# Performance work log

Measured on AMD Instinct MI355X. Metric: run time of the kernel, lower is better.

## Reference

```python
import jax, jax.numpy as jnp
import numpy as np

SEQ = 2048
D_MODEL = 2048
N_HEADS = 16
D_HEAD = D_MODEL // N_HEADS
GN_EPS = 1e-5


def apply_xpos(x, inv=False, base=10000.0, scale_base=512.0):
    # x: (sqlen, d_head). Standard xPos: rotary embedding with exponential length scale.
    s, d = x.shape
    half = d // 2
    freqs = 1.0 / (base ** (jnp.arange(half, dtype=jnp.float32) / half))
    pos = jnp.arange(s, dtype=jnp.float32)
    ang = pos[:, None] * freqs[None, :]                       # (s, half)
    sin, cos = jnp.sin(ang), jnp.cos(ang)
    scale = ((jnp.arange(half, dtype=jnp.float32) + 0.4 * d) / (1.4 * d)) ** (pos[:, None] / scale_base)
    if inv:
        scale = 1.0 / scale
    x1, x2 = x[:, :half], x[:, half:]
    y1 = (x1 * cos - x2 * sin) * scale
    y2 = (x1 * sin + x2 * cos) * scale
    return jnp.concatenate([y1, y2], axis=-1)


def setup_inputs() -> dict:
    key = jax.random.key(0)
    ks = jax.random.split(key, 8)
    s = D_MODEL ** -0.5
    return {
        "x": jax.random.normal(ks[0], (SEQ, D_MODEL), jnp.float32),
        "state": jax.random.normal(ks[1], (N_HEADS, D_HEAD, D_HEAD), jnp.float32) * 0.1,
        "Wqkv": jax.random.normal(ks[2], (3 * D_MODEL, D_MODEL), jnp.float32) * s,
        "Walpha": jax.random.normal(ks[3], (1, D_MODEL), jnp.float32) * s,
        "gn_w": jnp.ones((D_MODEL,), jnp.float32),
        "gn_b": jnp.zeros((D_MODEL,), jnp.float32),
        "Wgate": jax.random.normal(ks[4], (D_MODEL, D_MODEL), jnp.float32) * s,
        "Wout": jax.random.normal(ks[5], (D_MODEL, D_MODEL), jnp.float32) * s,
    }


def reference(x, state, Wqkv, Walpha, gn_w, gn_b, Wgate, Wout):
    sqlen = x.shape[0]
    # qkv projection -> (3, H, s, Dh)
    qkv = (x @ Wqkv.T).reshape(sqlen, 3, N_HEADS, D_HEAD).transpose(1, 2, 0, 3)
    q, k, v = qkv[0], qkv[1], qkv[2]
    q = jax.vmap(apply_xpos)(q)
    k = jax.vmap(lambda t: apply_xpos(t, inv=True))(k)

    alphas = -jnp.log1p(jnp.exp(-(x @ Walpha.T)))             # log-sigmoid, (s, 1)
    k = (1.0 - jnp.exp(alphas)) * k                            # broadcast (s,1) over (H,s,Dh)
    a = jnp.cumsum(alphas, axis=0)                             # (s, 1)

    # Decay matrix; mask BEFORE exp (equivalent to tril-after since upper is zeroed,
    # but avoids overflow in exp for the upper triangle).
    tril = jnp.tril(jnp.ones((sqlen, sqlen), bool))
    Delta = jnp.exp(jnp.where(tril, a - a.T, -jnp.inf))        # (s, s)

    attn = jnp.tril(jnp.einsum('hid,hjd,ij->hij', q, k, Delta))  # (H, s, s)
    ret = jnp.einsum('hij,hjd->ihd', attn, v)                    # (s, H, Dh)

    new_state = jnp.exp(a[-1]) * state                           # (H, Dh, Dh)
    ret = ret + jnp.einsum('hid,hde->ihe', q, new_state)
    new_state = new_state + jnp.einsum('hid,hie,i->hde', k, v, jnp.exp(a[::-1, 0]))

    # GroupNorm(n_heads groups) over d_model, per token
    r = ret.reshape(sqlen, N_HEADS, D_HEAD)
    mu = r.mean(-1, keepdims=True)
    var = r.var(-1, keepdims=True)
    r = (r - mu) * jax.lax.rsqrt(var + GN_EPS)
    ret = r.reshape(sqlen, D_MODEL) * gn_w + gn_b

    gate = jax.nn.swish(ret @ Wgate.T)
    out = (gate * ret) @ Wout.T
    return out, new_state
```

## Files before the change

kernel.cpp:

```cpp
#include <hip/hip_runtime.h>

#define SEQ 2048
#define DM 2048
#define NH 16
#define DH 128

typedef float f32x4 __attribute__((ext_vector_type(4)));
typedef short s16x8 __attribute__((ext_vector_type(8)));

__device__ __forceinline__ ushort f2bf(float f) {
    unsigned u = __builtin_bit_cast(unsigned, f);
    return (ushort)((u + 0x7FFFu + ((u >> 16) & 1u)) >> 16);
}
__device__ __forceinline__ float bf2f(ushort u) {
    return __builtin_bit_cast(float, (unsigned)u << 16);
}
__device__ __forceinline__ void gload_lds16(const void* g, void* l) {
    __builtin_amdgcn_global_load_lds((const __attribute__((address_space(1))) void*)g,
                                     (__attribute__((address_space(3))) void*)l, 16, 0, 0);
}

__global__ __launch_bounds__(256) void k_prep1(const float* __restrict__ x,
                                               const float* __restrict__ wal,
                                               ushort* __restrict__ x_bf,
                                               float* __restrict__ z,
                                               const float* __restrict__ Wqkv,
                                               ushort* __restrict__ Wqkv_bf,
                                               float* __restrict__ tsin,
                                               float* __restrict__ tcos,
                                               float* __restrict__ tsc) {
    int b = blockIdx.x, t = threadIdx.x;
    if (b < SEQ) {
        const float4* xr = (const float4*)(x + (size_t)b * DM);
        const float4* wa = (const float4*)wal;
        float4 v0 = xr[t], v1 = xr[t + 256];
        float4 w0 = wa[t], w1 = wa[t + 256];
        float s = v0.x * w0.x + v0.y * w0.y + v0.z * w0.z + v0.w * w0.w
                + v1.x * w1.x + v1.y * w1.y + v1.z * w1.z + v1.w * w1.w;
        ushort4 o0, o1;
        o0.x = f2bf(v0.x); o0.y = f2bf(v0.y); o0.z = f2bf(v0.z); o0.w = f2bf(v0.w);
        o1.x = f2bf(v1.x); o1.y = f2bf(v1.y); o1.z = f2bf(v1.z); o1.w = f2bf(v1.w);
        ushort4* xb = (ushort4*)(x_bf + (size_t)b * DM);
        xb[t] = o0; xb[t + 256] = o1;
        __shared__ float red[4];
        int lane = t & 63, wv = t >> 6;
        #pragma unroll
        for (int off = 32; off; off >>= 1) s += __shfl_down(s, off);
        if (lane == 0) red[wv] = s;
        __syncthreads();
        if (t == 0) z[b] = red[0] + red[1] + red[2] + red[3];
    } else if (b < SEQ + 3 * DM * DM / 4 / 256) {
        int i = (b - SEQ) * 256 + t;
        float4 v = ((const float4*)Wqkv)[i];
        ushort4 o;
        o.x = f2bf(v.x); o.y = f2bf(v.y); o.z = f2bf(v.z); o.w = f2bf(v.w);
        ((ushort4*)Wqkv_bf)[i] = o;
    } else {
        int idx = (b - SEQ - 3 * DM * DM / 4 / 256) * 256 + t;
        int i = idx >> 6, j = idx & 63;
        float freq = powf(10000.f, -(float)j / 64.f);
        float ang = (float)i * freq;
        tsin[idx] = sinf(ang);
        tcos[idx] = cosf(ang);
        tsc[idx]  = powf(((float)j + 51.2f) / 179.2f, (float)i / 512.f);
    }
}

__global__ __launch_bounds__(256) void k_scan(const float* __restrict__ z,
                                              float* __restrict__ a,
                                              float* __restrict__ wrev,
                                              float* __restrict__ kscale,
                                              float* __restrict__ exp_alast) {
    __shared__ float sh[SEQ];
    __shared__ float csum[256];
    int t = threadIdx.x;
    for (int i = t; i < SEQ; i += 256) {
        float al = -log1pf(expf(-z[i]));
        sh[i] = al;
        kscale[i] = 1.f - expf(al);
    }
    __syncthreads();
    int base = t * 8;
    float run = 0.f, loc[8];
    #pragma unroll
    for (int j = 0; j < 8; j++) { run += sh[base + j]; loc[j] = run; }
    csum[t] = run;
    __syncthreads();
    if (t == 0) {
        float r = 0.f;
        for (int i = 0; i < 256; i++) { float v = csum[i]; csum[i] = r; r += v; }
    }
    __syncthreads();
    float off = csum[t];
    #pragma unroll
    for (int j = 0; j < 8; j++) { float av = loc[j] + off; sh[base + j] = av; a[base + j] = av; }
    __syncthreads();
    for (int i = t; i < SEQ; i += 256) wrev[i] = expf(sh[SEQ - 1 - i]);
    if (t == 0) *exp_alast = expf(sh[SEQ - 1]);
}

template <int EPI, int STORE_BF16>
__global__ __launch_bounds__(256) void k_gemm_mfma(
    const ushort* __restrict__ A,
    const ushort* __restrict__ B,
    void* __restrict__ Cv, int ldc,
    const ushort* __restrict__ aux,
    int K)
{
    __shared__ __align__(16) ushort As[128 * 32];
    __shared__ __align__(16) ushort Bs[128 * 32];
    int bx = blockIdx.x, by = blockIdx.y;
    int nwg = gridDim.x * gridDim.y;
    if ((nwg & 7) == 0) {
        int id = by * gridDim.x + bx;
        int cpx = nwg >> 3;
        int swz = (id & 7) * cpx + (id >> 3);
        bx = swz % gridDim.x; by = swz / gridDim.x;
    }
    int bm = by * 128, bn = bx * 128;
    int tid = threadIdx.x;
    int w = tid >> 6, l = tid & 63;
    int wr = w >> 1, wc = w & 1;
    int lr = l & 15, kg = l >> 4;

    int srow = w * 16 + (l >> 2);
    int scol = (l & 3) * 8;
    const ushort* ga0 = A + (size_t)(bm + srow) * K + scol;
    const ushort* ga1 = A + (size_t)(bm + 64 + srow) * K + scol;
    const ushort* gb0 = B + (size_t)(bn + srow) * K + scol;
    const ushort* gb1 = B + (size_t)(bn + 64 + srow) * K + scol;
    ushort* la0 = As + w * 512;
    ushort* la1 = As + 2048 + w * 512;
    ushort* lb0 = Bs + w * 512;
    ushort* lb1 = Bs + 2048 + w * 512;

    f32x4 acc[4][4] = {};

    for (int k0 = 0; k0 < K; k0 += 32) {
        __syncthreads();
        gload_lds16(ga0 + k0, la0);
        gload_lds16(ga1 + k0, la1);
        gload_lds16(gb0 + k0, lb0);
        gload_lds16(gb1 + k0, lb1);
        __syncthreads();

        s16x8 af[4], bfr[4];
        #pragma unroll
        for (int m = 0; m < 4; m++)
            af[m] = *(const s16x8*)(As + (wr * 64 + m * 16 + lr) * 32 + kg * 8);
        #pragma unroll
        for (int n = 0; n < 4; n++)
            bfr[n] = *(const s16x8*)(Bs + (wc * 64 + n * 16 + lr) * 32 + kg * 8);
        #pragma unroll
        for (int m = 0; m < 4; m++)
            #pragma unroll
            for (int n = 0; n < 4; n++)
                asm volatile("v_mfma_f32_16x16x32_bf16 %0, %1, %2, %0"
                             : "+v"(acc[m][n]) : "v"(af[m]), "v"(bfr[n]));
    }
    asm volatile("s_nop 7\n\ts_nop 7\n\ts_nop 7" ::: );

    #pragma unroll
    for (int m = 0; m < 4; m++) {
        int grow = bm + wr * 64 + m * 16 + kg * 4;
        #pragma unroll
        for (int n = 0; n < 4; n++) {
            int gcol = bn + wc * 64 + n * 16 + lr;
            #pragma unroll
            for (int j = 0; j < 4; j++) {
                float c = acc[m][n][j];
                size_t off = (size_t)(grow + j) * ldc + gcol;
                if (EPI == 1) {
                    float sig = 1.f / (1.f + __expf(-c));
                    c = c * sig * bf2f(aux[off]);
                }
                if (STORE_BF16) ((ushort*)Cv)[off] = f2bf(c);
                else            ((float*)Cv)[off] = c;
            }
        }
    }
}

__global__ __launch_bounds__(256) void k_gemm_qkv(
    const ushort* __restrict__ A,
    const ushort* __restrict__ B,
    const float* __restrict__ tsin,
    const float* __restrict__ tcos,
    const float* __restrict__ tsc,
    const float* __restrict__ kscale,
    const float* __restrict__ wrev,
    ushort* __restrict__ qh,
    ushort* __restrict__ kh,
    ushort* __restrict__ vth,
    ushort* __restrict__ kwtr)
{
    __shared__ __align__(16) char smem[34816];
    ushort* As = (ushort*)smem;
    ushort* Bs = (ushort*)(smem + 8192);
    const int K = DM;
    int bx = blockIdx.x, by = blockIdx.y;
    {
        int id = by * gridDim.x + bx;
        int cpx = (gridDim.x * gridDim.y) >> 3;
        int swz = (id & 7) * cpx + (id >> 3);
        bx = swz % gridDim.x; by = swz / gridDim.x;
    }
    int bm = by * 128, bn = bx * 128;
    int tid = threadIdx.x;
    int w = tid >> 6, l = tid & 63;
    int wr = w >> 1, wc = w & 1;
    int lr = l & 15, kg = l >> 4;

    int srow = w * 16 + (l >> 2);
    int scol = (l & 3) * 8;
    const ushort* ga0 = A + (size_t)(bm + srow) * K + scol;
    const ushort* ga1 = A + (size_t)(bm + 64 + srow) * K + scol;
    const ushort* gb0 = B + (size_t)(bn + srow) * K + scol;
    const ushort* gb1 = B + (size_t)(bn + 64 + srow) * K + scol;
    ushort* la0 = As + w * 512;
    ushort* la1 = As + 2048 + w * 512;
    ushort* lb0 = Bs + w * 512;
    ushort* lb1 = Bs + 2048 + w * 512;

    f32x4 acc[4][4] = {};

    for (int k0 = 0; k0 < K; k0 += 32) {
        __syncthreads();
        gload_lds16(ga0 + k0, la0);
        gload_lds16(ga1 + k0, la1);
        gload_lds16(gb0 + k0, lb0);
        gload_lds16(gb1 + k0, lb1);
        __syncthreads();

        s16x8 af[4], bfr[4];
        #pragma unroll
        for (int m = 0; m < 4; m++)
            af[m] = *(const s16x8*)(As + (wr * 64 + m * 16 + lr) * 32 + kg * 8);
        #pragma unroll
        for (int n = 0; n < 4; n++)
            bfr[n] = *(const s16x8*)(Bs + (wc * 64 + n * 16 + lr) * 32 + kg * 8);
        #pragma unroll
        for (int m = 0; m < 4; m++)
            #pragma unroll
            for (int n = 0; n < 4; n++)
                asm volatile("v_mfma_f32_16x16x32_bf16 %0, %1, %2, %0"
                             : "+v"(acc[m][n]) : "v"(af[m]), "v"(bfr[n]));
    }
    asm volatile("s_nop 7\n\ts_nop 7\n\ts_nop 7" ::: );

    __syncthreads();
    ushort* S = (ushort*)smem;
    #pragma unroll
    for (int m = 0; m < 4; m++) {
        int row = wr * 64 + m * 16 + kg * 4;
        #pragma unroll
        for (int n = 0; n < 4; n++) {
            int col = wc * 64 + n * 16 + lr;
            #pragma unroll
            for (int j = 0; j < 4; j++)
                S[(row + j) * 129 + col] = f2bf(acc[m][n][j]);
        }
    }
    __syncthreads();

    int type = bn >> 11;
    int h = (bn & 2047) >> 7;

    if (type < 2) {
        #pragma unroll 4
        for (int rr = 0; rr < 32; rr++) {
            int r = w * 32 + rr;
            int i = bm + r;
            float sn = tsin[i * 64 + l], cs = tcos[i * 64 + l], sc = tsc[i * 64 + l];
            float v1 = bf2f(S[r * 129 + l]), v2 = bf2f(S[r * 129 + l + 64]);
            float r1 = v1 * cs - v2 * sn, r2 = v1 * sn + v2 * cs;
            size_t ob = ((size_t)h * SEQ + i) * DH;
            if (type == 0) {
                qh[ob + l]      = f2bf(r1 * sc);
                qh[ob + l + 64] = f2bf(r2 * sc);
            } else {
                float ks = kscale[i], wv = wrev[i];
                float isc = 1.f / sc;
                float k1 = r1 * isc * ks, k2 = r2 * isc * ks;
                kh[ob + l]      = f2bf(k1);
                kh[ob + l + 64] = f2bf(k2);
                S[r * 129 + l]      = f2bf(k1 * wv);
                S[r * 129 + l + 64] = f2bf(k2 * wv);
            }
        }
    }
    if (type >= 1) {
        __syncthreads();
        ushort* dstT = (type == 1) ? kwtr : vth;
        #pragma unroll 4
        for (int dd = 0; dd < 32; dd++) {
            int d = w * 32 + dd;
            ushort2 o;
            o.x = S[(2 * l) * 129 + d];
            o.y = S[(2 * l + 1) * 129 + d];
            *(ushort2*)(dstT + ((size_t)h * DH + d) * SEQ + bm + 2 * l) = o;
        }
    }
}

#define NUNITS 48
__constant__ unsigned char U_QT[NUNITS] = {
    31,31,30,15, 30,29,29,28,14, 28,27,27,26,13, 26,25,25,24,12,
    24,23,23,22,11, 22,21,21,20,10, 20,19,19,18,9, 18,17,17,16,8,
    16,7,6,5,4,3,2,1,0};
__constant__ unsigned char U_T0[NUNITS] = {
    0,16,0,0, 16,0,15,0,0, 15,0,14,0,0, 14,0,13,0,0,
    13,0,12,0,0, 12,0,11,0,0, 11,0,10,0,0, 10,0,9,0,0,
    9,0,0,0,0,0,0,0,0};
__constant__ unsigned char U_T1[NUNITS] = {
    16,32,16,16, 31,15,30,15,15, 29,14,28,14,14, 27,13,26,13,13,
    25,12,24,12,12, 23,11,22,11,11, 21,10,20,10,10, 19,9,18,9,9,
    17,8,7,6,5,4,3,2,1};

__global__ __launch_bounds__(256) void k_attn_mega(
    const ushort* __restrict__ qh,
    const ushort* __restrict__ kh,
    const ushort* __restrict__ vth,
    const ushort* __restrict__ kwtr,
    const float* __restrict__ a,
    float* __restrict__ ret,
    float* __restrict__ ret2,
    float* __restrict__ part,
    const float* __restrict__ Wgate,
    ushort* __restrict__ Wgate_bf,
    const float* __restrict__ Wout,
    ushort* __restrict__ Wout_bf)
{
    __shared__ __align__(16) char smem[81920];
    int h = blockIdx.x, u = blockIdx.y;
    int tid = threadIdx.x;
    int w = tid >> 6, l = tid & 63;
    int lr = l & 15, kg = l >> 4;

    if (u >= 56) {
        int id = (u - 56) * NH + h;
        const float4* g0 = (const float4*)Wgate;
        const float4* g1 = (const float4*)Wout;
        #pragma unroll 4
        for (int it = 0; it < 32; it++) {
            int idx = id * 8192 + it * 256 + tid;
            float4 v = g0[idx];
            ushort4 o;
            o.x = f2bf(v.x); o.y = f2bf(v.y); o.z = f2bf(v.z); o.w = f2bf(v.w);
            ((ushort4*)Wgate_bf)[idx] = o;
            v = g1[idx];
            o.x = f2bf(v.x); o.y = f2bf(v.y); o.z = f2bf(v.z); o.w = f2bf(v.w);
            ((ushort4*)Wout_bf)[idx] = o;
        }
        return;
    }
    if (u >= 48) {
        int ch = u - 48;
        const ushort* A = kwtr + (size_t)h * DH * SEQ + ch * (SEQ / 8);
        const ushort* B = vth  + (size_t)h * DH * SEQ + ch * (SEQ / 8);
        ushort* As = (ushort*)smem;
        ushort* Bs = (ushort*)(smem + 8192);
        int wr = w >> 1, wc = w & 1;
        int srow = w * 16 + (l >> 2);
        int scol = (l & 3) * 8;
        const ushort* ga0 = A + (size_t)srow * SEQ + scol;
        const ushort* ga1 = A + (size_t)(64 + srow) * SEQ + scol;
        const ushort* gb0 = B + (size_t)srow * SEQ + scol;
        const ushort* gb1 = B + (size_t)(64 + srow) * SEQ + scol;
        ushort* la0 = As + w * 512;
        ushort* la1 = As + 2048 + w * 512;
        ushort* lb0 = Bs + w * 512;
        ushort* lb1 = Bs + 2048 + w * 512;
        f32x4 acc[4][4] = {};
        for (int k0 = 0; k0 < SEQ / 8; k0 += 32) {
            __syncthreads();
            gload_lds16(ga0 + k0, la0);
            gload_lds16(ga1 + k0, la1);
            gload_lds16(gb0 + k0, lb0);
            gload_lds16(gb1 + k0, lb1);
            __syncthreads();
            s16x8 af[4], bfr[4];
            #pragma unroll
            for (int m = 0; m < 4; m++)
                af[m] = *(const s16x8*)(As + (wr * 64 + m * 16 + lr) * 32 + kg * 8);
            #pragma unroll
            for (int n = 0; n < 4; n++)
                bfr[n] = *(const s16x8*)(Bs + (wc * 64 + n * 16 + lr) * 32 + kg * 8);
            #pragma unroll
            for (int m = 0; m < 4; m++)
                #pragma unroll
                for (int n = 0; n < 4; n++)
                    asm volatile("v_mfma_f32_16x16x32_bf16 %0, %1, %2, %0"
                                 : "+v"(acc[m][n]) : "v"(af[m]), "v"(bfr[n]));
        }
        asm volatile("s_nop 7\n\ts_nop 7\n\ts_nop 7" ::: );
        float* p = part + ((size_t)ch * NH + h) * DH * DH;
        #pragma unroll
        for (int m = 0; m < 4; m++) {
            int grow = wr * 64 + m * 16 + kg * 4;
            #pragma unroll
            for (int n = 0; n < 4; n++) {
                int gcol = wc * 64 + n * 16 + lr;
                #pragma unroll
                for (int j = 0; j < 4; j++)
                    p[(size_t)(grow + j) * DH + gcol] = acc[m][n][j];
            }
        }
        return;
    }

    int qt = U_QT[u], t0 = U_T0[u], t1 = U_T1[u];
    int i0 = qt * 64;
    const ushort* Q  = qh  + (size_t)h * SEQ * DH;
    const ushort* K  = kh  + (size_t)h * SEQ * DH;
    const ushort* Vt = vth + (size_t)h * DH * SEQ;
#define KS(B) ((ushort*)(smem + (B) * 16384))
#define VS(B) ((ushort*)(smem + 32768 + (B) * 16384))
    char* Ps = smem + 65536;
    float* a_lds = (float*)(smem + 73728);

    int span = t1 * 64;
    for (int i = tid; i < span; i += 256) a_lds[i] = a[i];

    s16x8 qf[4];
    #pragma unroll
    for (int c = 0; c < 4; c++)
        qf[c] = *(const s16x8*)(Q + (size_t)(i0 + w * 16 + lr) * DH + c * 32 + kg * 8);
    float aq[4];
    #pragma unroll
    for (int r = 0; r < 4; r++) aq[r] = a[i0 + w * 16 + kg * 4 + r];

    f32x4 oacc[8] = {};

#define STAGE(T, B) do { int j0_ = (T) * 64;                                      \
    _Pragma("unroll") for (int g = 0; g < 4; g++) {                               \
        int row = w * 16 + g * 4 + (l >> 4);                                      \
        int cb = ((l & 15) * 16) ^ ((row & 7) << 4);                              \
        gload_lds16(K + (size_t)(j0_ + row) * DH + cb / 2,                        \
                    (char*)KS(B) + (w * 16 + g * 4) * 256); }                     \
    _Pragma("unroll") for (int g = 0; g < 4; g++) {                               \
        int e = w * 32 + g * 8 + (l >> 3);                                        \
        int cb = ((l & 7) * 16) ^ ((e & 7) << 4);                                 \
        gload_lds16(Vt + (size_t)e * SEQ + j0_ + cb / 2,                          \
                    (char*)VS(B) + (w * 32 + g * 8) * 128); }                     \
} while (0)

    STAGE(t0, 0);
    __syncthreads();

    for (int t = t0; t < t1; t++) {
        int cur = (t - t0) & 1;
        if (t + 1 < t1) {
            STAGE(t + 1, cur ^ 1);
            asm volatile("s_waitcnt vmcnt(8)" ::: "memory");
        } else {
            asm volatile("s_waitcnt vmcnt(0)" ::: "memory");
        }
        __builtin_amdgcn_s_barrier();

        f32x4 sacc[4] = {};
        __builtin_amdgcn_s_setprio(1);
        #pragma unroll
        for (int n = 0; n < 4; n++) {
            int krow = n * 16 + lr;
            #pragma unroll
            for (int c = 0; c < 4; c++) {
                s16x8 kf = *(const s16x8*)((const char*)KS(cur) + krow * 256 +
                            ((c * 64 + kg * 16) ^ ((krow & 7) << 4)));
                asm volatile("v_mfma_f32_16x16x32_bf16 %0, %1, %2, %0"
                             : "+v"(sacc[n]) : "v"(qf[c]), "v"(kf));
            }
        }
        __builtin_amdgcn_s_setprio(0);
        asm volatile("s_nop 7\n\ts_nop 7" ::: );

        int j0 = t * 64;
        float aref = a_lds[j0];
        float ei[4], ej[4];
        #pragma unroll
        for (int r = 0; r < 4; r++) ei[r] = __expf(aq[r] - aref);
        #pragma unroll
        for (int n = 0; n < 4; n++) ej[n] = __expf(aref - a_lds[j0 + n * 16 + lr]);
        bool diag = (t == qt);
        #pragma unroll
        for (int n = 0; n < 4; n++) {
            #pragma unroll
            for (int r = 0; r < 4; r++) {
                float wv = ei[r] * ej[n];
                if (diag)
                    wv = (n * 16 + lr <= w * 16 + kg * 4 + r) ? wv : 0.f;
                float p = sacc[n][r] * wv;
                int prow = w * 16 + kg * 4 + r;
                *(ushort*)(Ps + prow * 128 +
                           (((n * 16 + lr) * 2) ^ ((prow & 7) << 4))) = f2bf(p);
            }
        }
        __builtin_amdgcn_s_setprio(1);
        #pragma unroll
        for (int c2 = 0; c2 < 2; c2++) {
            int prow = w * 16 + lr;
            s16x8 pf = *(const s16x8*)((const char*)Ps + prow * 128 +
                        ((c2 * 64 + kg * 16) ^ ((prow & 7) << 4)));
            #pragma unroll
            for (int n2 = 0; n2 < 8; n2++) {
                int erow = n2 * 16 + lr;
                s16x8 vf = *(const s16x8*)((const char*)VS(cur) + erow * 128 +
                            ((c2 * 64 + kg * 16) ^ ((erow & 7) << 4)));
                asm volatile("v_mfma_f32_16x16x32_bf16 %0, %1, %2, %0"
                             : "+v"(oacc[n2]) : "v"(pf), "v"(vf));
            }
        }
        __builtin_amdgcn_s_setprio(0);
        asm volatile("s_waitcnt lgkmcnt(0)" ::: "memory");
        __builtin_amdgcn_s_barrier();
    }
#undef STAGE
    asm volatile("s_nop 7\n\ts_nop 7\n\ts_nop 7" ::: );

    float* dst = (t0 == 0) ? ret + (size_t)i0 * DM
                           : ret2 + (size_t)(i0 - 1024) * DM;
    #pragma unroll
    for (int n2 = 0; n2 < 8; n2++) {
        #pragma unroll
        for (int j = 0; j < 4; j++) {
            int ri = w * 16 + kg * 4 + j;
            dst[(size_t)ri * DM + h * DH + n2 * 16 + lr] = oacc[n2][j];
        }
    }
}

__global__ __launch_bounds__(64) void k_gnorm(const float* __restrict__ ret,
                                              const float* __restrict__ ret2,
                                              const float* __restrict__ gw,
                                              const float* __restrict__ gb,
                                              ushort* __restrict__ retn_bf,
                                              const float* __restrict__ part,
                                              const float* __restrict__ state,
                                              const float* __restrict__ exp_alast,
                                              float* __restrict__ out_state) {
    int i = blockIdx.x, h = blockIdx.y;
    int t = threadIdx.x;
    if (i >= SEQ) {
        int bx2 = i - SEQ;
        int idx4 = bx2 * 64 + t;
        size_t off = (size_t)h * (DH * DH / 4) + idx4;
        float ea = *exp_alast;
        float4 s4 = ((const float4*)state)[off];
        float4 acc;
        acc.x = s4.x * ea; acc.y = s4.y * ea; acc.z = s4.z * ea; acc.w = s4.w * ea;
        #pragma unroll
        for (int ch = 0; ch < 8; ch++) {
            float4 p4 = ((const float4*)part)[((size_t)ch * NH) * (DH * DH / 4) + off];
            acc.x += p4.x; acc.y += p4.y; acc.z += p4.z; acc.w += p4.w;
        }
        ((float4*)out_state)[off] = acc;
        return;
    }
    const float* r = ret + (size_t)i * DM + h * DH;
    float v0 = r[t], v1 = r[t + 64];
    if (i >= 1024) {
        const float* r2 = ret2 + (size_t)(i - 1024) * DM + h * DH;
        v0 += r2[t]; v1 += r2[t + 64];
    }
    float s = v0 + v1, sq = v0 * v0 + v1 * v1;
    #pragma unroll
    for (int off = 32; off; off >>= 1) { s += __shfl_xor(s, off); sq += __shfl_xor(sq, off); }
    float mu = s * (1.f / 128.f);
    float var = sq * (1.f / 128.f) - mu * mu;
    float inv = rsqrtf(var + 1e-5f);
    ushort* o = retn_bf + (size_t)i * DM + h * DH;
    o[t]      = f2bf((v0 - mu) * inv * gw[h * DH + t]      + gb[h * DH + t]);
    o[t + 64] = f2bf((v1 - mu) * inv * gw[h * DH + t + 64] + gb[h * DH + t + 64]);
}

extern "C" void kernel_launch(void* const* d_in, const int* in_sizes, int n_in,
                              void* d_out, int out_size, void* d_ws, size_t ws_size,
                              hipStream_t stream) {
    (void)in_sizes; (void)n_in; (void)out_size; (void)ws_size;
    const float* x      = (const float*)d_in[0];
    const float* state  = (const float*)d_in[1];
    const float* Wqkv   = (const float*)d_in[2];
    const float* Walpha = (const float*)d_in[3];
    const float* gn_w   = (const float*)d_in[4];
    const float* gn_b   = (const float*)d_in[5];
    const float* Wgate  = (const float*)d_in[6];
    const float* Wout   = (const float*)d_in[7];
    float* out       = (float*)d_out;
    float* out_state = out + (size_t)SEQ * DM;

    char* base = (char*)d_ws;
    ushort* x_bf     = (ushort*)base;
    ushort* retn_bf  = (ushort*)base;
    ushort* Wqkv_bf  = (ushort*)(base + 8388608);
    float*  ret      = (float*)(base + 8388608);
    float*  ret2     = (float*)(base + 25165824);
    ushort* qh       = (ushort*)(base + 33554432);
    ushort* kh       = (ushort*)(base + 41943040);
    ushort* vth      = (ushort*)(base + 50331648);
    ushort* kwtr     = (ushort*)(base + 58720256);
    float*  part     = (float*)(base + 67108864);
    ushort* gr_bf    = (ushort*)(base + 67108864);
    float*  tsin     = (float*)(base + 75497472);
    float*  tcos     = (float*)(base + 75497472 + 524288);
    float*  tsc      = (float*)(base + 75497472 + 1048576);
    ushort* Wgate_bf = (ushort*)(base + 75497472);
    ushort* Wout_bf  = (ushort*)(base + 83886080);
    float*  smalls   = (float*)(base + 92274688);
    float* z = smalls, *a = z + SEQ, *wrev = a + SEQ, *kscale = wrev + SEQ, *exp_alast = kscale + SEQ;

    k_prep1<<<dim3(SEQ + 3 * DM * DM / 4 / 256 + SEQ * 64 / 256), dim3(256), 0, stream>>>(
        x, Walpha, x_bf, z, Wqkv, Wqkv_bf, tsin, tcos, tsc);
    k_scan<<<dim3(1), dim3(256), 0, stream>>>(z, a, wrev, kscale, exp_alast);
    k_gemm_qkv<<<dim3(48, SEQ / 128), dim3(256), 0, stream>>>(
        x_bf, Wqkv_bf, tsin, tcos, tsc, kscale, wrev, qh, kh, vth, kwtr);
    k_attn_mega<<<dim3(NH, 64), dim3(256), 0, stream>>>(
        qh, kh, vth, kwtr, a, ret, ret2, part,
        Wgate, Wgate_bf, Wout, Wout_bf);
    k_gnorm<<<dim3(SEQ + 64, NH), dim3(64), 0, stream>>>(
        ret, ret2, gn_w, gn_b, retn_bf, part, state, exp_alast, out_state);
    k_gemm_mfma<1, 1><<<dim3(DM / 128, SEQ / 128), dim3(256), 0, stream>>>(
        retn_bf, Wgate_bf, gr_bf, DM, retn_bf, DM);
    k_gemm_mfma<0, 0><<<dim3(DM / 128, SEQ / 128), dim3(256), 0, stream>>>(
        gr_bf, Wout_bf, out, DM, nullptr, DM);
}
```

Baseline: 240.9 us.

## Double K-tile depth to 64 with XOR-swizzled LDS layout in GEMM kernels

Both GEMM kernels now stage 64-wide K slices per iteration instead of 32, halving the number of barrier pairs per output tile. The LDS layout uses an XOR swizzle on 16-byte chunks so the wider rows avoid bank conflicts on fragment reads. The generic kernel now hardcodes the stride as DM and ignores K, which is only correct if every caller passes K equal to DM. It also doubles LDS use in the generic kernel, which could reduce occupancy.

```diff
diff --git a/kernel.cpp b/kernel.cpp
--- a/kernel.cpp
+++ b/kernel.cpp
@@ -107,8 +107,9 @@
     const ushort* __restrict__ aux,
     int K)
 {
-    __shared__ __align__(16) ushort As[128 * 32];
-    __shared__ __align__(16) ushort Bs[128 * 32];
+    (void)K;
+    __shared__ __align__(16) ushort As[128 * 64];
+    __shared__ __align__(16) ushort Bs[128 * 64];
     int bx = blockIdx.x, by = blockIdx.y;
     int nwg = gridDim.x * gridDim.y;
     if ((nwg & 7) == 0) {
@@ -123,40 +124,44 @@
     int wr = w >> 1, wc = w & 1;
     int lr = l & 15, kg = l >> 4;
 
-    int srow = w * 16 + (l >> 2);
-    int scol = (l & 3) * 8;
-    const ushort* ga0 = A + (size_t)(bm + srow) * K + scol;
-    const ushort* ga1 = A + (size_t)(bm + 64 + srow) * K + scol;
-    const ushort* gb0 = B + (size_t)(bn + srow) * K + scol;
-    const ushort* gb1 = B + (size_t)(bn + 64 + srow) * K + scol;
-    ushort* la0 = As + w * 512;
-    ushort* la1 = As + 2048 + w * 512;
-    ushort* lb0 = Bs + w * 512;
-    ushort* lb1 = Bs + 2048 + w * 512;
+    int srow = w * 32 + (l >> 3);
+    int scol = ((l & 7) ^ (l >> 3)) * 8;
+    const ushort* ga = A + (size_t)(bm + srow) * DM + scol;
+    const ushort* gb = B + (size_t)(bn + srow) * DM + scol;
+    ushort* la = As + (w * 32) * 64;
+    ushort* lb = Bs + (w * 32) * 64;
 
     f32x4 acc[4][4] = {};
 
-    for (int k0 = 0; k0 < K; k0 += 32) {
+    for (int k0 = 0; k0 < DM; k0 += 64) {
         __syncthreads();
-        gload_lds16(ga0 + k0, la0);
-        gload_lds16(ga1 + k0, la1);
-        gload_lds16(gb0 + k0, lb0);
-        gload_lds16(gb1 + k0, lb1);
+        #pragma unroll
+        for (int g = 0; g < 4; g++) {
+            gload_lds16(ga + (size_t)(g * 8) * DM + k0, la + g * 8 * 64);
+            gload_lds16(gb + (size_t)(g * 8) * DM + k0, lb + g * 8 * 64);
+        }
         __syncthreads();
 
-        s16x8 af[4], bfr[4];
-        #pragma unroll
-        for (int m = 0; m < 4; m++)
-            af[m] = *(const s16x8*)(As + (wr * 64 + m * 16 + lr) * 32 + kg * 8);
-        #pragma unroll
-        for (int n = 0; n < 4; n++)
-            bfr[n] = *(const s16x8*)(Bs + (wc * 64 + n * 16 + lr) * 32 + kg * 8);
-        #pragma unroll
-        for (int m = 0; m < 4; m++)
-            #pragma unroll
-            for (int n = 0; n < 4; n++)
-                asm volatile("v_mfma_f32_16x16x32_bf16 %0, %1, %2, %0"
-                             : "+v"(acc[m][n]) : "v"(af[m]), "v"(bfr[n]));
+        #pragma unroll
+        for (int kk = 0; kk < 2; kk++) {
+            s16x8 af[4], bfr[4];
+            #pragma unroll
+            for (int m = 0; m < 4; m++) {
+                int row = wr * 64 + m * 16 + lr;
+                af[m] = *(const s16x8*)(As + row * 64 + (((kk * 4 + kg) ^ (lr & 7)) * 8));
+            }
+            #pragma unroll
+            for (int n = 0; n < 4; n++) {
+                int row = wc * 64 + n * 16 + lr;
+                bfr[n] = *(const s16x8*)(Bs + row * 64 + (((kk * 4 + kg) ^ (lr & 7)) * 8));
+            }
+            #pragma unroll
+            for (int m = 0; m < 4; m++)
+                #pragma unroll
+                for (int n = 0; n < 4; n++)
+                    asm volatile("v_mfma_f32_16x16x32_bf16 %0, %1, %2, %0"
+                                 : "+v"(acc[m][n]) : "v"(af[m]), "v"(bfr[n]));
+        }
     }
     asm volatile("s_nop 7\n\ts_nop 7\n\ts_nop 7" ::: );
 
@@ -194,10 +199,9 @@
     ushort* __restrict__ vth,
     ushort* __restrict__ kwtr)
 {
-    __shared__ __align__(16) char smem[34816];
+    __shared__ __align__(16) char smem[33024];
     ushort* As = (ushort*)smem;
-    ushort* Bs = (ushort*)(smem + 8192);
-    const int K = DM;
+    ushort* Bs = (ushort*)(smem + 16384);
     int bx = blockIdx.x, by = blockIdx.y;
     {
         int id = by * gridDim.x + bx;
@@ -211,40 +215,44 @@
     int wr = w >> 1, wc = w & 1;
     int lr = l & 15, kg = l >> 4;
 
-    int srow = w * 16 + (l >> 2);
-    int scol = (l & 3) * 8;
-    const ushort* ga0 = A + (size_t)(bm + srow) * K + scol;
-    const ushort* ga1 = A + (size_t)(bm + 64 + srow) * K + scol;
-    const ushort* gb0 = B + (size_t)(bn + srow) * K + scol;
-    const ushort* gb1 = B + (size_t)(bn + 64 + srow) * K + scol;
-    ushort* la0 = As + w * 512;
-    ushort* la1 = As + 2048 + w * 512;
-    ushort* lb0 = Bs + w * 512;
-    ushort* lb1 = Bs + 2048 + w * 512;
+    int srow = w * 32 + (l >> 3);
+    int scol = ((l & 7) ^ (l >> 3)) * 8;
+    const ushort* ga = A + (size_t)(bm + srow) * DM + scol;
+    const ushort* gb = B + (size_t)(bn + srow) * DM + scol;
+    ushort* la = As + (w * 32) * 64;
+    ushort* lb = Bs + (w * 32) * 64;
 
     f32x4 acc[4][4] = {};
 
-    for (int k0 = 0; k0 < K; k0 += 32) {
+    for (int k0 = 0; k0 < DM; k0 += 64) {
         __syncthreads();
-        gload_lds16(ga0 + k0, la0);
-        gload_lds16(ga1 + k0, la1);
-        gload_lds16(gb0 + k0, lb0);
-        gload_lds16(gb1 + k0, lb1);
+        #pragma unroll
+        for (int g = 0; g < 4; g++) {
+            gload_lds16(ga + (size_t)(g * 8) * DM + k0, la + g * 8 * 64);
+            gload_lds16(gb + (size_t)(g * 8) * DM + k0, lb + g * 8 * 64);
+        }
         __syncthreads();
 
-        s16x8 af[4], bfr[4];
-        #pragma unroll
-        for (int m = 0; m < 4; m++)
-            af[m] = *(const s16x8*)(As + (wr * 64 + m * 16 + lr) * 32 + kg * 8);
-        #pragma unroll
-        for (int n = 0; n < 4; n++)
-            bfr[n] = *(const s16x8*)(Bs + (wc * 64 + n * 16 + lr) * 32 + kg * 8);
-        #pragma unroll
-        for (int m = 0; m < 4; m++)
-            #pragma unroll
-            for (int n = 0; n < 4; n++)
-                asm volatile("v_mfma_f32_16x16x32_bf16 %0, %1, %2, %0"
-                             : "+v"(acc[m][n]) : "v"(af[m]), "v"(bfr[n]));
+        #pragma unroll
+        for (int kk = 0; kk < 2; kk++) {
+            s16x8 af[4], bfr[4];
+            #pragma unroll
+            for (int m = 0; m < 4; m++) {
+                int row = wr * 64 + m * 16 + lr;
+                af[m] = *(const s16x8*)(As + row * 64 + (((kk * 4 + kg) ^ (lr & 7)) * 8));
+            }
+            #pragma unroll
+            for (int n = 0; n < 4; n++) {
+                int row = wc * 64 + n * 16 + lr;
+                bfr[n] = *(const s16x8*)(Bs + row * 64 + (((kk * 4 + kg) ^ (lr & 7)) * 8));
+            }
+            #pragma unroll
+            for (int m = 0; m < 4; m++)
+                #pragma unroll
+                for (int n = 0; n < 4; n++)
+                    asm volatile("v_mfma_f32_16x16x32_bf16 %0, %1, %2, %0"
+                                 : "+v"(acc[m][n]) : "v"(af[m]), "v"(bfr[n]));
+        }
     }
     asm volatile("s_nop 7\n\ts_nop 7\n\ts_nop 7" ::: );
 
```

New measurement: 231.3 us. -4.0%, faster.
